# Optimization experiments

Measured on AMD Instinct MI355X. Metric: run time of the kernel, lower is better.

## Reference

```python
import jax, jax.numpy as jnp
import numpy as np

EMBED = 1024
HEADS = 16
HEAD_DIM = EMBED // HEADS


def setup_inputs() -> dict:
    key = jax.random.key(0)
    ks = jax.random.split(key, 12)
    N, S, E = 4, 2048, EMBED
    scale = 1.0 / np.sqrt(E)
    inp = {
        "values": jax.random.normal(ks[0], (N, S, E), dtype=jnp.float32),
        "keys": jax.random.normal(ks[1], (N, S, E), dtype=jnp.float32),
        "query": jax.random.normal(ks[2], (N, S, E), dtype=jnp.float32),
        "mask": jnp.ones((N, 1, 1, S), dtype=jnp.int32),
        # Linear params: y = x @ W + b (W stored as [in, out])
        "Wv": jax.random.normal(ks[3], (E, E), dtype=jnp.float32) * scale,
        "bv": jnp.zeros((E,), dtype=jnp.float32),
        "Wk": jax.random.normal(ks[4], (E, E), dtype=jnp.float32) * scale,
        "bk": jnp.zeros((E,), dtype=jnp.float32),
        "Wq": jax.random.normal(ks[5], (E, E), dtype=jnp.float32) * scale,
        "bq": jnp.zeros((E,), dtype=jnp.float32),
        "Wo": jax.random.normal(ks[6], (E, E), dtype=jnp.float32) * scale,
        "bo": jnp.zeros((E,), dtype=jnp.float32),
    }
    return inp


def reference(values, keys, query, mask, Wv, bv, Wk, bk, Wq, bq, Wo, bo):
    N, Q, E = query.shape
    V = values.shape[1]
    K = keys.shape[1]
    v = (values @ Wv + bv).reshape(N, V, HEADS, HEAD_DIM)
    k = (keys @ Wk + bk).reshape(N, K, HEADS, HEAD_DIM)
    q = (query @ Wq + bq).reshape(N, Q, HEADS, HEAD_DIM)
    # energy: [N, H, Q, K]
    energy = jnp.einsum("nqhd,nkhd->nhqk", q, k)
    energy = jnp.where(mask == 0, jnp.float32(-1e20), energy)
    # NOTE: original scales by sqrt(embed_size), not sqrt(head_dim)
    attn = jax.nn.softmax(energy / jnp.sqrt(jnp.float32(E)), axis=3)
    out = jnp.einsum("nhql,nlhd->nqhd", attn, v).reshape(N, Q, E)
    return out @ Wo + bo
```

## Files before the change

kernel.cpp:

```cpp
#include <hip/hip_runtime.h>

#define H 16
#define DH 64
#define S 2048
#define E 1024
#define NB 4

typedef short short8_t __attribute__((ext_vector_type(8)));
typedef short short4_t __attribute__((ext_vector_type(4)));
typedef float float4_t __attribute__((ext_vector_type(4)));

__device__ inline unsigned short f2bf(float f) {
    union { float f; unsigned u; } v; v.f = f;
    unsigned r = v.u + 0x7fffu + ((v.u >> 16) & 1u);
    return (unsigned short)(r >> 16);
}

__device__ __forceinline__ unsigned pk_bf16(float a, float b) {
    union { float f; unsigned u; } ua, ub;
    ua.f = a; ub.f = b;
    unsigned ra = ua.u + 0x7fffu + ((ua.u >> 16) & 1u);
    unsigned rb = ub.u + 0x7fffu + ((ub.u >> 16) & 1u);
    return __builtin_amdgcn_perm(rb, ra, 0x07060302u);
}

__device__ __forceinline__ unsigned cvt_pk_bf16(float a, float b) {
    unsigned r;
    asm("v_cvt_pk_bf16_f32 %0, %1, %2" : "=v"(r) : "v"(a), "v"(b));
    return r;
}

__device__ __forceinline__ float4_t mfma16x16x16_bf16(short4_t a, short4_t b, float4_t c) {
#if __has_builtin(__builtin_amdgcn_mfma_f32_16x16x16bf16_1k)
    return __builtin_amdgcn_mfma_f32_16x16x16bf16_1k(a, b, c, 0, 0, 0);
#else
    float4_t d;
    asm("v_mfma_f32_16x16x16_bf16 %0, %1, %2, %3" : "=v"(d) : "v"(a), "v"(b), "v"(c));
    return d;
#endif
}

__device__ __forceinline__ void async_copy16(const unsigned short* g, unsigned short* l) {
    __builtin_amdgcn_global_load_lds(
        (const __attribute__((address_space(1))) unsigned int*)g,
        (__attribute__((address_space(3))) unsigned int*)l, 16, 0, 0);
}

__global__ __launch_bounds__(256) void xcvt_kernel(
    const float* __restrict__ v, const float* __restrict__ k,
    const float* __restrict__ q, unsigned short* __restrict__ xv,
    unsigned short* __restrict__ xk, unsigned short* __restrict__ xq)
{
    const int z = blockIdx.y;
    const float* src = (z == 0) ? v : (z == 1) ? k : q;
    unsigned short* dst = (z == 0) ? xv : (z == 1) ? xk : xq;
    size_t i0 = ((size_t)blockIdx.x * 256 + threadIdx.x) * 8;
    float4 f0 = *reinterpret_cast<const float4*>(src + i0);
    float4 f1 = *reinterpret_cast<const float4*>(src + i0 + 4);
    uint4 o;
    o.x = pk_bf16(f0.x, f0.y); o.y = pk_bf16(f0.z, f0.w);
    o.z = pk_bf16(f1.x, f1.y); o.w = pk_bf16(f1.z, f1.w);
    *reinterpret_cast<uint4*>(dst + i0) = o;
}

__global__ __launch_bounds__(256) void wcvt_kernel(
    const float* __restrict__ Wv, const float* __restrict__ Wk,
    const float* __restrict__ Wq, const float* __restrict__ Wo,
    unsigned short* __restrict__ Wt)
{
    __shared__ float tile[64][65];
    const float* W = (blockIdx.z == 0) ? Wv : (blockIdx.z == 1) ? Wk
                   : (blockIdx.z == 2) ? Wq : Wo;
    unsigned short* out = Wt + (size_t)blockIdx.z * (E * E);
    const int k0 = blockIdx.x * 64, n0 = blockIdx.y * 64;
    const int tid = threadIdx.x;
#pragma unroll
    for (int i = 0; i < 4; ++i) {
        int c = i * 256 + tid;
        int kl = c >> 4, nl4 = (c & 15) * 4;
        float4 v = *reinterpret_cast<const float4*>(W + (size_t)(k0 + kl) * E + n0 + nl4);
        tile[kl][nl4 + 0] = v.x; tile[kl][nl4 + 1] = v.y;
        tile[kl][nl4 + 2] = v.z; tile[kl][nl4 + 3] = v.w;
    }
    __syncthreads();
#pragma unroll
    for (int i = 0; i < 4; ++i) {
        int c = i * 256 + tid;
        int nl = c >> 4, kl4 = (c & 15) * 4;
        ushort4 o;
        o.x = f2bf(tile[kl4 + 0][nl]); o.y = f2bf(tile[kl4 + 1][nl]);
        o.z = f2bf(tile[kl4 + 2][nl]); o.w = f2bf(tile[kl4 + 3][nl]);
        *reinterpret_cast<ushort4*>(out + (size_t)(n0 + nl) * E + k0 + kl4) = o;
    }
}

template<int MODE>
__global__ __launch_bounds__(256) void proj_kernel(
    const unsigned short* __restrict__ A, const unsigned short* __restrict__ WT,
    const float* __restrict__ bias, unsigned short* __restrict__ out)
{
    __shared__ __align__(16) unsigned short As[2][128][64];
    __shared__ __align__(16) unsigned short Bs[2][128][64];

    const int tid = threadIdx.x;
    const int m0 = blockIdx.y * 128;
    const int n0 = blockIdx.x * 128;
    const int wave = tid >> 6, lane = tid & 63;
    const int wm = wave >> 1, wn = wave & 1;
    const int quad = lane >> 4, l16 = lane & 15;
    const int r8 = lane >> 3;
    const int c8 = (lane & 7) ^ (r8 & 7);

    float4_t acc[4][4];
#pragma unroll
    for (int i = 0; i < 4; ++i)
#pragma unroll
        for (int j = 0; j < 4; ++j) { float4_t z = {0.f,0.f,0.f,0.f}; acc[i][j] = z; }

#pragma unroll
    for (int j = 0; j < 4; ++j) {
        int row = wave * 32 + j * 8 + r8;
        async_copy16(A  + (size_t)(m0 + row) * E + c8 * 8, &As[0][wave * 32 + j * 8][0]);
        async_copy16(WT + (size_t)(n0 + row) * E + c8 * 8, &Bs[0][wave * 32 + j * 8][0]);
    }

    for (int it = 0; it < 16; ++it) {
        const int cur = it & 1, nxt = cur ^ 1;
        __syncthreads();

        if (it < 15) {
            const int kn = (it + 1) * 64;
#pragma unroll
            for (int j = 0; j < 4; ++j) {
                int row = wave * 32 + j * 8 + r8;
                async_copy16(A  + (size_t)(m0 + row) * E + kn + c8 * 8, &As[nxt][wave * 32 + j * 8][0]);
                async_copy16(WT + (size_t)(n0 + row) * E + kn + c8 * 8, &Bs[nxt][wave * 32 + j * 8][0]);
            }
        }
#pragma unroll
        for (int kk = 0; kk < 2; ++kk) {
            short8_t a[4], b[4];
#pragma unroll
            for (int mi = 0; mi < 4; ++mi)
                a[mi] = *reinterpret_cast<const short8_t*>(
                    &As[cur][wm * 64 + mi * 16 + l16][((kk * 4 + quad) ^ (l16 & 7)) * 8]);
#pragma unroll
            for (int nj = 0; nj < 4; ++nj)
                b[nj] = *reinterpret_cast<const short8_t*>(
                    &Bs[cur][wn * 64 + nj * 16 + l16][((kk * 4 + quad) ^ (l16 & 7)) * 8]);
#pragma unroll
            for (int x = 0; x < 4; ++x)
#pragma unroll
                for (int y = 0; y < 4; ++y) {
                    if (MODE == 0)
                        acc[x][y] = __builtin_amdgcn_mfma_f32_16x16x32_bf16(b[x], a[y], acc[x][y], 0, 0, 0);
                    else
                        acc[x][y] = __builtin_amdgcn_mfma_f32_16x16x32_bf16(a[x], b[y], acc[x][y], 0, 0, 0);
                }
        }
    }

    if (MODE == 0) {
#pragma unroll
        for (int x = 0; x < 4; ++x) {
            float4 bb = *reinterpret_cast<const float4*>(&bias[n0 + wn * 64 + x * 16 + quad * 4]);
#pragma unroll
            for (int y = 0; y < 4; ++y) {
                int m = m0 + wm * 64 + y * 16 + l16;
                int nn = m >> 11, s = m & 2047;
#pragma unroll
                for (int r = 0; r < 4; ++r) {
                    int gcol = n0 + wn * 64 + x * 16 + quad * 4 + r;
                    int h = gcol >> 6, d = gcol & 63;
                    float val = acc[x][y][r] + ((const float*)&bb)[r];
                    out[(((size_t)(nn * H + h)) * DH + d) * S + s] = f2bf(val);
                }
            }
        }
    } else {
#pragma unroll
        for (int x = 0; x < 4; ++x) {
#pragma unroll
            for (int y = 0; y < 4; ++y) {
                int gcol = n0 + wn * 64 + y * 16 + l16;
                float bvv = bias[gcol];
                int h = gcol >> 6, d = gcol & 63;
#pragma unroll
                for (int r = 0; r < 4; ++r) {
                    int gm = m0 + wm * 64 + x * 16 + quad * 4 + r;
                    float val = acc[x][y][r] + bvv;
                    int nn = gm >> 11, s = gm & 2047;
                    out[(((size_t)(nn * H + h)) * S + s) * DH + d] = f2bf(val);
                }
            }
        }
    }
}

__global__ __launch_bounds__(512, 8) void flash_kernel(
    const unsigned short* __restrict__ Qb, const unsigned short* __restrict__ Kb,
    const unsigned short* __restrict__ VTb, const int* __restrict__ mask,
    unsigned short* __restrict__ AO)
{
    __shared__ __align__(16) unsigned short Ks[2][64][64];
    __shared__ __align__(16) unsigned short Vs[2][64][64];
    __shared__ float am[2][64];
    __shared__ float lbuf[8][16];

    const int tid = threadIdx.x;
    const int wave = tid >> 6, lane = tid & 63;
    const int quad = lane >> 4, l16 = lane & 15;
    const int r8 = lane >> 3;
    const int c8 = (lane & 7) ^ (r8 & 7);
    const int sw = wave & 3;

    const int wlin = blockIdx.y * 16 + blockIdx.x;
    const int wid = (wlin & 7) * 128 + (wlin >> 3);
    const int qt = wid & 15;
    const int nh = wid >> 4;
    const int n = nh >> 4, h = nh & 15;
    const size_t hb = (size_t)nh * S * DH;
    const unsigned short* Qh = Qb + hb;
    const unsigned short* Kh = Kb + hb;
    const unsigned short* Vh = VTb + hb;
    const int* mp = mask + n * S;

    const float c1 = 0.03125f * 1.4426950408889634f;
    const float C2_UNMASK = -23.083120654223414f;
    const float C2_MASK   = -1.44e20f;

    short8_t qa[2];
#pragma unroll
    for (int kk = 0; kk < 2; ++kk) {
        int row = qt * 128 + wave * 16 + l16;
        qa[kk] = *reinterpret_cast<const short8_t*>(Qh + (size_t)row * DH + kk * 32 + quad * 8);
    }

    float4_t o[4];
#pragma unroll
    for (int nj = 0; nj < 4; ++nj) { float4_t z = {0.f,0.f,0.f,0.f}; o[nj] = z; }
    float lsum = 0.f;

#pragma unroll
    for (int j = 0; j < 2; ++j) {
        int row = sw * 16 + j * 8 + r8;
        if (wave < 4) async_copy16(Kh + (size_t)row * DH + c8 * 8, &Ks[0][sw * 16 + j * 8][0]);
        else          async_copy16(Vh + (size_t)row * S + c8 * 8,  &Vs[0][sw * 16 + j * 8][0]);
    }
    if (tid < 64) am[0][tid] = (mp[tid] == 0) ? C2_MASK : C2_UNMASK;

    for (int it = 0; it < 32; ++it) {
        const int cur = it & 1, nxt = cur ^ 1;
        __syncthreads();

        const int kn = (it < 31) ? (it + 1) * 64 : 0;
#pragma unroll
        for (int j = 0; j < 2; ++j) {
            int row = sw * 16 + j * 8 + r8;
            if (wave < 4) async_copy16(Kh + (size_t)(kn + row) * DH + c8 * 8, &Ks[nxt][sw * 16 + j * 8][0]);
            else          async_copy16(Vh + (size_t)row * S + kn + c8 * 8,    &Vs[nxt][sw * 16 + j * 8][0]);
        }
        if (tid < 64) am[nxt][tid] = (mp[kn + tid] == 0) ? C2_MASK : C2_UNMASK;

        float4_t st[4];
#pragma unroll
        for (int kvb = 0; kvb < 4; ++kvb) { float4_t z = {0.f,0.f,0.f,0.f}; st[kvb] = z; }
        __builtin_amdgcn_s_setprio(1);
#pragma unroll
        for (int kk = 0; kk < 2; ++kk) {
            short8_t ak[4];
#pragma unroll
            for (int kvb = 0; kvb < 4; ++kvb)
                ak[kvb] = *reinterpret_cast<const short8_t*>(
                    &Ks[cur][kvb * 16 + l16][((kk * 4 + quad) ^ (l16 & 7)) * 8]);
#pragma unroll
            for (int kvb = 0; kvb < 4; ++kvb)
                st[kvb] = __builtin_amdgcn_mfma_f32_16x16x32_bf16(ak[kvb], qa[kk], st[kvb], 0, 0, 0);
        }
        __builtin_amdgcn_s_setprio(0);

        unsigned pw[4][2];
#pragma unroll
        for (int kvb = 0; kvb < 4; ++kvb) {
            float4 c2v = *reinterpret_cast<const float4*>(&am[cur][kvb * 16 + quad * 4]);
            float p0 = __builtin_amdgcn_exp2f(st[kvb][0] * c1 + c2v.x);
            float p1 = __builtin_amdgcn_exp2f(st[kvb][1] * c1 + c2v.y);
            float p2 = __builtin_amdgcn_exp2f(st[kvb][2] * c1 + c2v.z);
            float p3 = __builtin_amdgcn_exp2f(st[kvb][3] * c1 + c2v.w);
            lsum += (p0 + p1) + (p2 + p3);
            pw[kvb][0] = cvt_pk_bf16(p0, p1);
            pw[kvb][1] = cvt_pk_bf16(p2, p3);
        }

        const int vcol = (quad & 1) * 4;
        __builtin_amdgcn_s_setprio(1);
#pragma unroll
        for (int kvb = 0; kvb < 4; ++kvb) {
            const int vch = ((kvb * 2 + (quad >> 1)) ^ (l16 & 7)) * 8 + vcol;
            short4_t vb[4];
#pragma unroll
            for (int nj = 0; nj < 4; ++nj)
                vb[nj] = *reinterpret_cast<const short4_t*>(&Vs[cur][nj * 16 + l16][vch]);
            union { unsigned u[2]; short4_t s; } pu;
            pu.u[0] = pw[kvb][0]; pu.u[1] = pw[kvb][1];
#pragma unroll
            for (int nj = 0; nj < 4; ++nj)
                o[nj] = mfma16x16x16_bf16(pu.s, vb[nj], o[nj]);
        }
        __builtin_amdgcn_s_setprio(0);
    }

    lsum += __shfl_xor(lsum, 16); lsum += __shfl_xor(lsum, 32);
    if (lane < 16) lbuf[wave][lane] = lsum;

    float4 lv = *reinterpret_cast<const float4*>(&lbuf[wave][quad * 4]);
#pragma unroll
    for (int r = 0; r < 4; ++r) {
        float invl = __builtin_amdgcn_rcpf(((const float*)&lv)[r]);
        int qrow = qt * 128 + wave * 16 + quad * 4 + r;
        size_t gm = (size_t)n * S + qrow;
#pragma unroll
        for (int nj = 0; nj < 4; ++nj) {
            int col = h * DH + nj * 16 + l16;
            AO[gm * E + col] = f2bf(o[nj][r] * invl);
        }
    }
}

__global__ __launch_bounds__(256) void ogemm_kernel(
    const unsigned short* __restrict__ A, const unsigned short* __restrict__ WT,
    const float* __restrict__ bias, float* __restrict__ out)
{
    __shared__ __align__(16) unsigned short As[2][128][64];
    __shared__ __align__(16) unsigned short Bs[2][128][64];

    const int tid = threadIdx.x;
    const int m0 = blockIdx.y * 128;
    const int n0 = blockIdx.x * 128;
    const int wave = tid >> 6, lane = tid & 63;
    const int wm = wave >> 1, wn = wave & 1;
    const int quad = lane >> 4, l16 = lane & 15;
    const int r8 = lane >> 3;
    const int c8 = (lane & 7) ^ (r8 & 7);

    float4_t acc[4][4];
#pragma unroll
    for (int i = 0; i < 4; ++i)
#pragma unroll
        for (int j = 0; j < 4; ++j) { float4_t z = {0.f,0.f,0.f,0.f}; acc[i][j] = z; }

#pragma unroll
    for (int j = 0; j < 4; ++j) {
        int row = wave * 32 + j * 8 + r8;
        async_copy16(A  + (size_t)(m0 + row) * E + c8 * 8, &As[0][wave * 32 + j * 8][0]);
        async_copy16(WT + (size_t)(n0 + row) * E + c8 * 8, &Bs[0][wave * 32 + j * 8][0]);
    }

    for (int it = 0; it < 16; ++it) {
        const int cur = it & 1, nxt = cur ^ 1;
        __syncthreads();

        if (it < 15) {
            const int kn = (it + 1) * 64;
#pragma unroll
            for (int j = 0; j < 4; ++j) {
                int row = wave * 32 + j * 8 + r8;
                async_copy16(A  + (size_t)(m0 + row) * E + kn + c8 * 8, &As[nxt][wave * 32 + j * 8][0]);
                async_copy16(WT + (size_t)(n0 + row) * E + kn + c8 * 8, &Bs[nxt][wave * 32 + j * 8][0]);
            }
        }
#pragma unroll
        for (int kk = 0; kk < 2; ++kk) {
            short8_t a[4], b[4];
#pragma unroll
            for (int mi = 0; mi < 4; ++mi)
                a[mi] = *reinterpret_cast<const short8_t*>(
                    &As[cur][wm * 64 + mi * 16 + l16][((kk * 4 + quad) ^ (l16 & 7)) * 8]);
#pragma unroll
            for (int nj = 0; nj < 4; ++nj)
                b[nj] = *reinterpret_cast<const short8_t*>(
                    &Bs[cur][wn * 64 + nj * 16 + l16][((kk * 4 + quad) ^ (l16 & 7)) * 8]);
#pragma unroll
            for (int mi = 0; mi < 4; ++mi)
#pragma unroll
                for (int nj = 0; nj < 4; ++nj)
                    acc[mi][nj] = __builtin_amdgcn_mfma_f32_16x16x32_bf16(a[mi], b[nj], acc[mi][nj], 0, 0, 0);
        }
    }
#pragma unroll
    for (int mi = 0; mi < 4; ++mi)
#pragma unroll
        for (int nj = 0; nj < 4; ++nj) {
            int gcol = n0 + wn * 64 + nj * 16 + l16;
            float bvv = bias[gcol];
#pragma unroll
            for (int r = 0; r < 4; ++r) {
                int gm = m0 + wm * 64 + mi * 16 + quad * 4 + r;
                out[(size_t)gm * E + gcol] = acc[mi][nj][r] + bvv;
            }
        }
}

extern "C" void kernel_launch(void* const* d_in, const int* in_sizes, int n_in,
                              void* d_out, int out_size, void* d_ws, size_t ws_size,
                              hipStream_t stream) {
    const float* values = (const float*)d_in[0];
    const float* keys   = (const float*)d_in[1];
    const float* query  = (const float*)d_in[2];
    const int*   mask   = (const int*)d_in[3];
    const float* Wv = (const float*)d_in[4];  const float* bv = (const float*)d_in[5];
    const float* Wk = (const float*)d_in[6];  const float* bk = (const float*)d_in[7];
    const float* Wq = (const float*)d_in[8];  const float* bq = (const float*)d_in[9];
    const float* Wo = (const float*)d_in[10]; const float* bo = (const float*)d_in[11];
    float* out = (float*)d_out;

    char* ws = (char*)d_ws;
    unsigned short* Wt = (unsigned short*)ws;
    unsigned short* xv = (unsigned short*)(ws + 8388608);
    unsigned short* xk = (unsigned short*)(ws + 25165824);
    unsigned short* xq = (unsigned short*)(ws + 41943040);
    unsigned short* vt = (unsigned short*)(ws + 58720256);
    unsigned short* kb = xv;
    unsigned short* qb = xk;
    unsigned short* ao = xq;

    xcvt_kernel<<<dim3(4096, 3), 256, 0, stream>>>(values, keys, query, xv, xk, xq);
    wcvt_kernel<<<dim3(16, 16, 4), 256, 0, stream>>>(Wv, Wk, Wq, Wo, Wt);
    proj_kernel<0><<<dim3(8, 64), 256, 0, stream>>>(xv, Wt,           bv, vt);
    proj_kernel<1><<<dim3(8, 64), 256, 0, stream>>>(xk, Wt + 1048576, bk, kb);
    proj_kernel<1><<<dim3(8, 64), 256, 0, stream>>>(xq, Wt + 2097152, bq, qb);
    flash_kernel<<<dim3(16, 64), 512, 0, stream>>>(qb, kb, vt, mask, ao);
    ogemm_kernel<<<dim3(8, 64), 256, 0, stream>>>(ao, Wt + 3145728, bo, out);
}
```

Baseline: 401.1 us.

## Switch flash attention to 32x32x16 MFMA with 4 waves of 32 query rows

Rewrites the flash attention kernel to use 32x32x16 bf16 MFMA instead of 16x16 shapes, with each of 4 waves owning 32 query rows instead of 8 waves with 16 rows each. K/V tile loads are now issued by every wave, and the softmax, P·V fragment packing and output writeback are remapped to the 32x32 accumulator layout. The intent is to raise MFMA throughput per instruction and get more reuse of LDS reads, at the cost of more registers per wave and fewer waves per block to hide latency.

```diff
diff --git a/kernel.cpp b/kernel.cpp
--- a/kernel.cpp
+++ b/kernel.cpp
@@ -7,8 +7,8 @@
 #define NB 4
 
 typedef short short8_t __attribute__((ext_vector_type(8)));
-typedef short short4_t __attribute__((ext_vector_type(4)));
 typedef float float4_t __attribute__((ext_vector_type(4)));
+typedef float float16_t __attribute__((ext_vector_type(16)));
 
 __device__ inline unsigned short f2bf(float f) {
     union { float f; unsigned u; } v; v.f = f;
@@ -30,14 +30,8 @@
     return r;
 }
 
-__device__ __forceinline__ float4_t mfma16x16x16_bf16(short4_t a, short4_t b, float4_t c) {
-#if __has_builtin(__builtin_amdgcn_mfma_f32_16x16x16bf16_1k)
-    return __builtin_amdgcn_mfma_f32_16x16x16bf16_1k(a, b, c, 0, 0, 0);
-#else
-    float4_t d;
-    asm("v_mfma_f32_16x16x16_bf16 %0, %1, %2, %3" : "=v"(d) : "v"(a), "v"(b), "v"(c));
-    return d;
-#endif
+__device__ __forceinline__ float16_t mfma32(short8_t a, short8_t b, float16_t c) {
+    return __builtin_amdgcn_mfma_f32_32x32x16_bf16(a, b, c, 0, 0, 0);
 }
 
 __device__ __forceinline__ void async_copy16(const unsigned short* g, unsigned short* l) {
@@ -197,22 +191,21 @@
     }
 }
 
-__global__ __launch_bounds__(512, 8) void flash_kernel(
+__global__ __launch_bounds__(256, 4) void flash_kernel(
     const unsigned short* __restrict__ Qb, const unsigned short* __restrict__ Kb,
     const unsigned short* __restrict__ VTb, const int* __restrict__ mask,
     unsigned short* __restrict__ AO)
 {
     __shared__ __align__(16) unsigned short Ks[2][64][64];
     __shared__ __align__(16) unsigned short Vs[2][64][64];
-    __shared__ float am[2][64];
-    __shared__ float lbuf[8][16];
+    __shared__ __align__(16) float am[2][64];
+    __shared__ __align__(16) float lbuf[4][32];
 
     const int tid = threadIdx.x;
     const int wave = tid >> 6, lane = tid & 63;
-    const int quad = lane >> 4, l16 = lane & 15;
+    const int l32 = lane & 31, hf = lane >> 5;
     const int r8 = lane >> 3;
     const int c8 = (lane & 7) ^ (r8 & 7);
-    const int sw = wave & 3;
 
     const int wlin = blockIdx.y * 16 + blockIdx.x;
     const int wid = (wlin & 7) * 128 + (wlin >> 3);
@@ -229,23 +222,25 @@
     const float C2_UNMASK = -23.083120654223414f;
     const float C2_MASK   = -1.44e20f;
 
-    short8_t qa[2];
-#pragma unroll
-    for (int kk = 0; kk < 2; ++kk) {
-        int row = qt * 128 + wave * 16 + l16;
-        qa[kk] = *reinterpret_cast<const short8_t*>(Qh + (size_t)row * DH + kk * 32 + quad * 8);
-    }
-
-    float4_t o[4];
-#pragma unroll
-    for (int nj = 0; nj < 4; ++nj) { float4_t z = {0.f,0.f,0.f,0.f}; o[nj] = z; }
+    short8_t qa[4];
+#pragma unroll
+    for (int ks = 0; ks < 4; ++ks) {
+        int row = qt * 128 + wave * 32 + l32;
+        qa[ks] = *reinterpret_cast<const short8_t*>(Qh + (size_t)row * DH + ks * 16 + hf * 8);
+    }
+
+    float16_t o[2];
+#pragma unroll
+    for (int nb = 0; nb < 2; ++nb)
+#pragma unroll
+        for (int i = 0; i < 16; ++i) o[nb][i] = 0.f;
     float lsum = 0.f;
 
 #pragma unroll
     for (int j = 0; j < 2; ++j) {
-        int row = sw * 16 + j * 8 + r8;
-        if (wave < 4) async_copy16(Kh + (size_t)row * DH + c8 * 8, &Ks[0][sw * 16 + j * 8][0]);
-        else          async_copy16(Vh + (size_t)row * S + c8 * 8,  &Vs[0][sw * 16 + j * 8][0]);
+        int row = wave * 16 + j * 8 + r8;
+        async_copy16(Kh + (size_t)row * DH + c8 * 8, &Ks[0][wave * 16 + j * 8][0]);
+        async_copy16(Vh + (size_t)row * S + c8 * 8,  &Vs[0][wave * 16 + j * 8][0]);
     }
     if (tid < 64) am[0][tid] = (mp[tid] == 0) ? C2_MASK : C2_UNMASK;
 
@@ -256,73 +251,78 @@
         const int kn = (it < 31) ? (it + 1) * 64 : 0;
 #pragma unroll
         for (int j = 0; j < 2; ++j) {
-            int row = sw * 16 + j * 8 + r8;
-            if (wave < 4) async_copy16(Kh + (size_t)(kn + row) * DH + c8 * 8, &Ks[nxt][sw * 16 + j * 8][0]);
-            else          async_copy16(Vh + (size_t)row * S + kn + c8 * 8,    &Vs[nxt][sw * 16 + j * 8][0]);
+            int row = wave * 16 + j * 8 + r8;
+            async_copy16(Kh + (size_t)(kn + row) * DH + c8 * 8, &Ks[nxt][wave * 16 + j * 8][0]);
+            async_copy16(Vh + (size_t)row * S + kn + c8 * 8,    &Vs[nxt][wave * 16 + j * 8][0]);
         }
         if (tid < 64) am[nxt][tid] = (mp[kn + tid] == 0) ? C2_MASK : C2_UNMASK;
 
-        float4_t st[4];
-#pragma unroll
-        for (int kvb = 0; kvb < 4; ++kvb) { float4_t z = {0.f,0.f,0.f,0.f}; st[kvb] = z; }
+        unsigned w[2][4][2];
+#pragma unroll
+        for (int kvb = 0; kvb < 2; ++kvb) {
+            float16_t st;
+#pragma unroll
+            for (int i = 0; i < 16; ++i) st[i] = 0.f;
+            __builtin_amdgcn_s_setprio(1);
+#pragma unroll
+            for (int ks = 0; ks < 4; ++ks) {
+                short8_t ak = *reinterpret_cast<const short8_t*>(
+                    &Ks[cur][kvb * 32 + l32][((ks * 2 + hf) ^ (l32 & 7)) * 8]);
+                st = mfma32(ak, qa[ks], st);
+            }
+            __builtin_amdgcn_s_setprio(0);
+#pragma unroll
+            for (int g = 0; g < 4; ++g) {
+                float4 c2v = *reinterpret_cast<const float4*>(&am[cur][kvb * 32 + g * 8 + hf * 4]);
+                float p0 = __builtin_amdgcn_exp2f(st[g * 4 + 0] * c1 + c2v.x);
+                float p1 = __builtin_amdgcn_exp2f(st[g * 4 + 1] * c1 + c2v.y);
+                float p2 = __builtin_amdgcn_exp2f(st[g * 4 + 2] * c1 + c2v.z);
+                float p3 = __builtin_amdgcn_exp2f(st[g * 4 + 3] * c1 + c2v.w);
+                lsum += (p0 + p1) + (p2 + p3);
+                w[kvb][g][0] = cvt_pk_bf16(p0, p1);
+                w[kvb][g][1] = cvt_pk_bf16(p2, p3);
+            }
+        }
+
         __builtin_amdgcn_s_setprio(1);
 #pragma unroll
-        for (int kk = 0; kk < 2; ++kk) {
-            short8_t ak[4];
-#pragma unroll
-            for (int kvb = 0; kvb < 4; ++kvb)
-                ak[kvb] = *reinterpret_cast<const short8_t*>(
-                    &Ks[cur][kvb * 16 + l16][((kk * 4 + quad) ^ (l16 & 7)) * 8]);
-#pragma unroll
-            for (int kvb = 0; kvb < 4; ++kvb)
-                st[kvb] = __builtin_amdgcn_mfma_f32_16x16x32_bf16(ak[kvb], qa[kk], st[kvb], 0, 0, 0);
+        for (int ks2 = 0; ks2 < 4; ++ks2) {
+            const int kvb = ks2 >> 1, t = ks2 & 1;
+            union { unsigned u[4]; short8_t s; } pu;
+            pu.u[0] = w[kvb][t * 2][0];     pu.u[1] = w[kvb][t * 2][1];
+            pu.u[2] = w[kvb][t * 2 + 1][0]; pu.u[3] = w[kvb][t * 2 + 1][1];
+#pragma unroll
+            for (int nb = 0; nb < 2; ++nb) {
+                const int d = nb * 32 + l32;
+                uint2 v0 = *reinterpret_cast<const uint2*>(
+                    &Vs[cur][d][(((kvb * 4 + t * 2)     ) ^ (d & 7)) * 8 + hf * 4]);
+                uint2 v1 = *reinterpret_cast<const uint2*>(
+                    &Vs[cur][d][(((kvb * 4 + t * 2 + 1) ) ^ (d & 7)) * 8 + hf * 4]);
+                union { unsigned u[4]; short8_t s; } vu;
+                vu.u[0] = v0.x; vu.u[1] = v0.y; vu.u[2] = v1.x; vu.u[3] = v1.y;
+                o[nb] = mfma32(pu.s, vu.s, o[nb]);
+            }
         }
         __builtin_amdgcn_s_setprio(0);
-
-        unsigned pw[4][2];
-#pragma unroll
-        for (int kvb = 0; kvb < 4; ++kvb) {
-            float4 c2v = *reinterpret_cast<const float4*>(&am[cur][kvb * 16 + quad * 4]);
-            float p0 = __builtin_amdgcn_exp2f(st[kvb][0] * c1 + c2v.x);
-            float p1 = __builtin_amdgcn_exp2f(st[kvb][1] * c1 + c2v.y);
-            float p2 = __builtin_amdgcn_exp2f(st[kvb][2] * c1 + c2v.z);
-            float p3 = __builtin_amdgcn_exp2f(st[kvb][3] * c1 + c2v.w);
-            lsum += (p0 + p1) + (p2 + p3);
-            pw[kvb][0] = cvt_pk_bf16(p0, p1);
-            pw[kvb][1] = cvt_pk_bf16(p2, p3);
-        }
-
-        const int vcol = (quad & 1) * 4;
-        __builtin_amdgcn_s_setprio(1);
-#pragma unroll
-        for (int kvb = 0; kvb < 4; ++kvb) {
-            const int vch = ((kvb * 2 + (quad >> 1)) ^ (l16 & 7)) * 8 + vcol;
-            short4_t vb[4];
-#pragma unroll
-            for (int nj = 0; nj < 4; ++nj)
-                vb[nj] = *reinterpret_cast<const short4_t*>(&Vs[cur][nj * 16 + l16][vch]);
-            union { unsigned u[2]; short4_t s; } pu;
-            pu.u[0] = pw[kvb][0]; pu.u[1] = pw[kvb][1];
-#pragma unroll
-            for (int nj = 0; nj < 4; ++nj)
-                o[nj] = mfma16x16x16_bf16(pu.s, vb[nj], o[nj]);
-        }
-        __builtin_amdgcn_s_setprio(0);
-    }
-
-    lsum += __shfl_xor(lsum, 16); lsum += __shfl_xor(lsum, 32);
-    if (lane < 16) lbuf[wave][lane] = lsum;
-
-    float4 lv = *reinterpret_cast<const float4*>(&lbuf[wave][quad * 4]);
-#pragma unroll
-    for (int r = 0; r < 4; ++r) {
-        float invl = __builtin_amdgcn_rcpf(((const float*)&lv)[r]);
-        int qrow = qt * 128 + wave * 16 + quad * 4 + r;
-        size_t gm = (size_t)n * S + qrow;
-#pragma unroll
-        for (int nj = 0; nj < 4; ++nj) {
-            int col = h * DH + nj * 16 + l16;
-            AO[gm * E + col] = f2bf(o[nj][r] * invl);
+    }
+
+    lsum += __shfl_xor(lsum, 32);
+    if (lane < 32) lbuf[wave][lane] = lsum;
+
+#pragma unroll
+    for (int g = 0; g < 4; ++g) {
+        float4 dn = *reinterpret_cast<const float4*>(&lbuf[wave][g * 8 + hf * 4]);
+#pragma unroll
+        for (int r = 0; r < 4; ++r) {
+            float invl = __builtin_amdgcn_rcpf(((const float*)&dn)[r]);
+            int row = g * 8 + hf * 4 + r;
+            int qrow = qt * 128 + wave * 32 + row;
+            size_t gm = (size_t)n * S + qrow;
+#pragma unroll
+            for (int nb = 0; nb < 2; ++nb) {
+                int col = h * DH + nb * 32 + l32;
+                AO[gm * E + col] = f2bf(o[nb][g * 4 + r] * invl);
+            }
         }
     }
 }
@@ -429,6 +429,6 @@
     proj_kernel<0><<<dim3(8, 64), 256, 0, stream>>>(xv, Wt,           bv, vt);
     proj_kernel<1><<<dim3(8, 64), 256, 0, stream>>>(xk, Wt + 1048576, bk, kb);
     proj_kernel<1><<<dim3(8, 64), 256, 0, stream>>>(xq, Wt + 2097152, bq, qb);
-    flash_kernel<<<dim3(16, 64), 512, 0, stream>>>(qb, kb, vt, mask, ao);
+    flash_kernel<<<dim3(16, 64), 256, 0, stream>>>(qb, kb, vt, mask, ao);
     ogemm_kernel<<<dim3(8, 64), 256, 0, stream>>>(ao, Wt + 3145728, bo, out);
 }
```

Measured after the change: 351.2 us. 1.14x faster.
